# Kernel tuning notes

Measured on AMD Instinct MI355X. Metric: run time of the kernel, lower is better.

The kernel has to match this reference:

```python
import jax, jax.numpy as jnp
import numpy as np

B, DIM, T = 16, 128, 4096
CODEBOOK = 1024


def setup_inputs() -> dict:
    key = jax.random.key(0)
    k1, k2 = jax.random.split(key)
    x = jax.random.normal(k1, (B, DIM, T), dtype=jnp.float32)
    embed = jax.random.normal(k2, (CODEBOOK, DIM), dtype=jnp.float32) * 0.02
    return {"x": x, "embed": embed}


def reference(x, embed):
    Bq, D, Tq = x.shape
    n_codes = embed.shape[0]
    # [B, D, T] -> [B*T, D]
    x_flat = x.transpose(0, 2, 1).reshape(-1, D)
    d2 = (
        jnp.sum(x_flat * x_flat, axis=-1, keepdims=True)
        - 2.0 * (x_flat @ embed.T)
        + jnp.sum(embed * embed, axis=-1)[None, :]
    )  # [N, n_codes]
    indices = jnp.argmin(d2, axis=-1)  # [N]
    quantized = embed[indices]  # [N, D]
    # commitment_loss + codebook_loss: numerically both equal mse(x, q) in fwd
    diff = x_flat - quantized
    loss = 2.0 * jnp.mean(diff * diff)
    # straight-through value equals quantized in forward
    quantized_st = quantized.reshape(Bq, Tq, D).transpose(0, 2, 1)
    # utilization = fraction of codes used (jit-safe scatter instead of unique)
    used = jnp.zeros((n_codes,), jnp.float32).at[indices].set(1.0)
    utilization = jnp.sum(used) / n_codes
    return quantized_st, indices, loss, utilization
```

## Files before the change

kernel.cpp:

```cpp
#include <hip/hip_runtime.h>
#include <hip/hip_fp16.h>

#define B_ 16
#define D_ 128
#define T_ 4096
#define C_ 1024
#define N_ (B_*T_)
#define MARGIN 1.5e-3f

typedef __attribute__((ext_vector_type(8))) __fp16 fp16x8;
typedef __attribute__((ext_vector_type(4))) float f32x4;
typedef unsigned int u32;
typedef unsigned short u16;

static __device__ __forceinline__ fp16x8 as_fp16x8(int4 v) {
    union { int4 i; fp16x8 h; } u; u.i = v; return u.h;
}
static __device__ __forceinline__ u32 pack_h2(float a, float b) {
    return (u32)__half_as_ushort(__float2half(a)) |
           ((u32)__half_as_ushort(__float2half(b)) << 16);
}

__global__ __launch_bounds__(256) void vq_init_kernel(float* used, float* accum, int* nflag) {
    int tid = blockIdx.x * 256 + threadIdx.x;
    if (tid < C_) used[tid] = 0.0f;
    if (tid == 0) { accum[0] = 0.0f; nflag[0] = 0; }
}

__global__ __launch_bounds__(256) void vq_e2_kernel(const float* __restrict__ embed,
                                                    float* __restrict__ e2) {
#pragma clang fp contract(off)
    int c = blockIdx.x * 256 + threadIdx.x;
    const float* row = embed + (size_t)c * D_;
    float r[8];
#pragma unroll
    for (int j = 0; j < 8; ++j) { float v = row[j]; r[j] = v * v; }
    for (int i = 8; i < D_; i += 8) {
#pragma unroll
        for (int j = 0; j < 8; ++j) { float v = row[i + j]; r[j] = r[j] + v * v; }
    }
    e2[c] = ((r[0] + r[1]) + (r[2] + r[3])) + ((r[4] + r[5]) + (r[6] + r[7]));
}

__global__ __launch_bounds__(256) void vq_eprep_kernel(const float* __restrict__ embed,
                                                       u32* __restrict__ epk_hi,
                                                       u32* __restrict__ epk_lo,
                                                       float* __restrict__ eT) {
    int i = blockIdx.x * 256 + threadIdx.x;
    int c = i >> 6, d2 = i & 63;
    float2 v = reinterpret_cast<const float2*>(embed)[i];
    __half h0 = __float2half(v.x), h1 = __float2half(v.y);
    float l0 = v.x - __half2float(h0), l1 = v.y - __half2float(h1);
    u32 hp = (u32)__half_as_ushort(h0) | ((u32)__half_as_ushort(h1) << 16);
    u32 lp = (u32)__half_as_ushort(__float2half(l0)) |
             ((u32)__half_as_ushort(__float2half(l1)) << 16);
    int chunk = (c >> 6) * 16 + ((c >> 4) & 3) * 4 + (d2 >> 4);
    int oi = chunk * 256 + (((d2 >> 2) & 3) * 16 + (c & 15)) * 4 + (d2 & 3);
    epk_hi[oi] = hp;
    epk_lo[oi] = lp;
    int d0 = d2 * 2;
    eT[(size_t)d0 * C_ + c]       = v.x;
    eT[(size_t)(d0 + 1) * C_ + c] = v.y;
}

__global__ __launch_bounds__(256) void vq_mfma_kernel(
    const float* __restrict__ x, const u32* __restrict__ epk_hi, const u32* __restrict__ epk_lo,
    const float* __restrict__ e2, float* __restrict__ idx_f, int* __restrict__ idx_i,
    int* __restrict__ flagged, int* __restrict__ nflag)
{
    __shared__ int4  xb_lds[1024];
    __shared__ float mv1[4][64];
    __shared__ int   mi1[4][64];
    __shared__ float mv2[4][64];

    const int g  = blockIdx.x;
    const int b  = g >> 6;
    const int t0 = (g & 63) << 6;
    const int tid = threadIdx.x;
    const int w  = tid >> 6;
    const int l  = tid & 63;
    const int r  = l & 15;
    const int q  = l >> 4;

    {
        const int s = w;
        const float* xp = x + (size_t)b * ((size_t)D_ * T_) + (t0 + 16 * s + r);
#pragma unroll
        for (int t = 0; t < 4; ++t) {
            float f[8];
#pragma unroll
            for (int j = 0; j < 8; ++j)
                f[j] = xp[(size_t)(32 * t + 8 * q + j) * T_];
            int4 pk;
            pk.x = (int)pack_h2(f[0], f[1]);
            pk.y = (int)pack_h2(f[2], f[3]);
            pk.z = (int)pack_h2(f[4], f[5]);
            pk.w = (int)pack_h2(f[6], f[7]);
            xb_lds[(s * 4 + t) * 64 + l] = pk;
        }
    }
    __syncthreads();

    float rv1[4], rv2[4];
    int   ri1[4];
#pragma unroll
    for (int s = 0; s < 4; ++s) { rv1[s] = 3.4e38f; rv2[s] = 3.4e38f; ri1[s] = 0; }

    const u32* ephi = epk_hi + w * 1024 + l * 4;
    const u32* eplo = epk_lo + w * 1024 + l * 4;

    for (int rnd = 0; rnd < 16; ++rnd) {
        int4 eh4[4], el4[4];
#pragma unroll
        for (int t = 0; t < 4; ++t) {
            eh4[t] = *reinterpret_cast<const int4*>(ephi + rnd * 4096 + t * 256);
            el4[t] = *reinterpret_cast<const int4*>(eplo + rnd * 4096 + t * 256);
        }
        f32x4 eev = *reinterpret_cast<const f32x4*>(e2 + rnd * 64 + w * 16 + 4 * q);

#pragma unroll
        for (int s = 0; s < 4; ++s) {
            f32x4 acc = {0.f, 0.f, 0.f, 0.f};
#pragma unroll
            for (int t = 0; t < 4; ++t) {
                fp16x8 xa = as_fp16x8(xb_lds[(s * 4 + t) * 64 + l]);
                acc = __builtin_amdgcn_mfma_f32_16x16x32_f16(as_fp16x8(eh4[t]), xa, acc, 0, 0, 0);
                acc = __builtin_amdgcn_mfma_f32_16x16x32_f16(as_fp16x8(el4[t]), xa, acc, 0, 0, 0);
            }
#pragma unroll
            for (int reg = 0; reg < 4; ++reg) {
                float sc = fmaf(-2.0f, acc[reg], eev[reg]);
                int c = rnd * 64 + w * 16 + 4 * q + reg;
                if (sc < rv1[s]) { rv2[s] = rv1[s]; rv1[s] = sc; ri1[s] = c; }
                else rv2[s] = fminf(rv2[s], sc);
            }
        }
    }

#pragma unroll
    for (int s = 0; s < 4; ++s) {
        float v1 = rv1[s], v2 = rv2[s];
        int   i1 = ri1[s];
#pragma unroll
        for (int mo = 0; mo < 2; ++mo) {
            int m = 16 << mo;
            float ov1 = __shfl_xor(v1, m, 64);
            int   oi1 = __shfl_xor(i1, m, 64);
            float ov2 = __shfl_xor(v2, m, 64);
            float nv2 = fminf(fmaxf(v1, ov1), fminf(v2, ov2));
            if (ov1 < v1 || (ov1 == v1 && oi1 < i1)) { v1 = ov1; i1 = oi1; }
            v2 = nv2;
        }
        if (q == 0) { mv1[w][16 * s + r] = v1; mi1[w][16 * s + r] = i1; mv2[w][16 * s + r] = v2; }
    }
    __syncthreads();

    if (tid < 64) {
        float V1 = 3.4e38f, V2 = 3.4e38f;
        int   I1 = 0;
#pragma unroll
        for (int w2 = 0; w2 < 4; ++w2) {
            float a1 = mv1[w2][tid]; int ai = mi1[w2][tid]; float a2 = mv2[w2][tid];
            if (a1 < V1 || (a1 == V1 && ai < I1)) { V2 = fminf(V2, V1); V1 = a1; I1 = ai; }
            else V2 = fminf(V2, a1);
            V2 = fminf(V2, a2);
        }
        int n = g * 64 + tid;
        idx_i[n] = I1;
        idx_f[n] = (float)I1;
        if (V2 - V1 < MARGIN) { int pos = atomicAdd(nflag, 1); flagged[pos] = n; }
    }
}

__global__ __launch_bounds__(256) void vq_refine_kernel(
    const float* __restrict__ x, const float* __restrict__ eT,
    const float* __restrict__ e2,
    const int* __restrict__ flagged, const int* __restrict__ nflag,
    float* __restrict__ idx_f, int* __restrict__ idx_i)
{
    __shared__ float xs[D_];
    __shared__ float r8s[8];
    __shared__ float xxsh;
    __shared__ float wvv[4];
    __shared__ int   wvi[4];

    const int tid = threadIdx.x;
    const int wv_ = tid >> 6;
    const int l   = tid & 63;
    const int total = *nflag;

    for (int fi = blockIdx.x; fi < total; fi += gridDim.x) {
        __syncthreads();
        int n = flagged[fi];
        int b = n >> 12;
        int t = n & (T_ - 1);
        if (tid < D_) xs[tid] = x[(size_t)b * ((size_t)D_ * T_) + (size_t)tid * T_ + t];
        __syncthreads();

        if (tid < 8) {
#pragma clang fp contract(off)
            float v0 = xs[tid];
            float rj = v0 * v0;
            for (int i = 8; i < D_; i += 8) { float v = xs[i + tid]; rj = rj + v * v; }
            r8s[tid] = rj;
        }
        __syncthreads();
        if (tid == 0) {
#pragma clang fp contract(off)
            xxsh = ((r8s[0] + r8s[1]) + (r8s[2] + r8s[3])) + ((r8s[4] + r8s[5]) + (r8s[6] + r8s[7]));
        }
        __syncthreads();
        const float xx = xxsh;

        float acc0 = 0.f, acc1 = 0.f, acc2 = 0.f, acc3 = 0.f;
        const float* ep = eT + wv_ * 256 + l;
        for (int d = 0; d < D_; ++d) {
            float xv = xs[d];
            const float* rowp = ep + (size_t)d * C_;
            acc0 = fmaf(xv, rowp[0],   acc0);
            acc1 = fmaf(xv, rowp[64],  acc1);
            acc2 = fmaf(xv, rowp[128], acc2);
            acc3 = fmaf(xv, rowp[192], acc3);
        }

        float best = 3.4e38f;
        int   bi = 0;
        float a4[4] = {acc0, acc1, acc2, acc3};
#pragma unroll
        for (int k = 0; k < 4; ++k) {
            int c = wv_ * 256 + 64 * k + l;
            float s;
            {
#pragma clang fp contract(off)
                s = (xx - 2.0f * a4[k]) + e2[c];
            }
            if (s < best) { best = s; bi = c; }
        }
#pragma unroll
        for (int m = 1; m <= 32; m <<= 1) {
            float ov = __shfl_xor(best, m, 64);
            int   oc = __shfl_xor(bi, m, 64);
            if (ov < best || (ov == best && oc < bi)) { best = ov; bi = oc; }
        }
        if (l == 0) { wvv[wv_] = best; wvi[wv_] = bi; }
        __syncthreads();
        if (tid == 0) {
            float V = wvv[0]; int I = wvi[0];
#pragma unroll
            for (int w2 = 1; w2 < 4; ++w2) {
                if (wvv[w2] < V || (wvv[w2] == V && wvi[w2] < I)) { V = wvv[w2]; I = wvi[w2]; }
            }
            idx_i[n] = I;
            idx_f[n] = (float)I;
        }
    }
}

__global__ __launch_bounds__(256) void vq_gather_kernel(
    const float* __restrict__ x, const float* __restrict__ embed,
    const int* __restrict__ idx_i, float* __restrict__ out_q,
    float* __restrict__ accum, float* __restrict__ used)
{
    __shared__ int sidx[64];
    __shared__ float red[256];

    const int g  = blockIdx.x;
    const int b  = g >> 6;
    const int t0 = (g & 63) << 6;
    const int tid = threadIdx.x;

    if (tid < 64) {
        int ci = idx_i[g * 64 + tid];
        sidx[tid] = ci;
        used[ci] = 1.0f;
    }
    __syncthreads();

    const float* xb = x     + (size_t)b * ((size_t)D_ * T_) + t0;
    float*       ob = out_q + (size_t)b * ((size_t)D_ * T_) + t0;

    float local = 0.f;
#pragma unroll
    for (int k = 0; k < 32; ++k) {
        int e = tid + 256 * k;
        int d = e >> 6, tt = e & 63;
        float qv = embed[(size_t)sidx[tt] * D_ + d];
        float xv = xb[(size_t)d * T_ + tt];
        ob[(size_t)d * T_ + tt] = qv;
        float df = xv - qv;
        local += df * df;
    }

    red[tid] = local;
    __syncthreads();
    for (int st = 128; st > 0; st >>= 1) {
        if (tid < st) red[tid] += red[tid + st];
        __syncthreads();
    }
    if (tid == 0) atomicAdd(accum, red[0]);
}

__global__ __launch_bounds__(256) void vq_final_kernel(
    const float* __restrict__ used, const float* __restrict__ accum,
    float* __restrict__ out_loss, float* __restrict__ out_util)
{
    __shared__ float red[256];
    int tid = threadIdx.x;
    float s = 0.f;
    for (int k = tid; k < C_; k += 256) s += used[k];
    red[tid] = s;
    __syncthreads();
    for (int st = 128; st > 0; st >>= 1) {
        if (tid < st) red[tid] += red[tid + st];
        __syncthreads();
    }
    if (tid == 0) {
        out_loss[0] = 2.0f * accum[0] / (float)((size_t)N_ * D_);
        out_util[0] = red[0] / (float)C_;
    }
}

extern "C" void kernel_launch(void* const* d_in, const int* in_sizes, int n_in,
                              void* d_out, int out_size, void* d_ws, size_t ws_size,
                              hipStream_t stream) {
    const float* x     = (const float*)d_in[0];
    const float* embed = (const float*)d_in[1];

    float* out      = (float*)d_out;
    float* out_q    = out;
    float* idx_f    = out + (size_t)B_ * D_ * T_;
    float* out_loss = idx_f + N_;
    float* out_util = out_loss + 1;

    float* ws      = (float*)d_ws;
    float* e2      = ws;
    float* used    = ws + 1024;
    int*   idx_i   = (int*)(ws + 2048);
    float* accum   = ws + 67584;
    int*   nflag   = (int*)(ws + 67585);
    int*   flagged = (int*)(ws + 67588);
    u32*   epk_hi  = (u32*)(ws + 133124);
    u32*   epk_lo  = (u32*)(ws + 198660);
    float* eT      = ws + 264196;

    vq_init_kernel  <<<4, 256, 0, stream>>>(used, accum, nflag);
    vq_e2_kernel    <<<C_ / 256, 256, 0, stream>>>(embed, e2);
    vq_eprep_kernel <<<C_ * D_ / 2 / 256, 256, 0, stream>>>(embed, epk_hi, epk_lo, eT);
    vq_mfma_kernel  <<<N_ / 64, 256, 0, stream>>>(x, epk_hi, epk_lo, e2, idx_f, idx_i, flagged, nflag);
    vq_refine_kernel<<<1024, 256, 0, stream>>>(x, eT, e2, flagged, nflag, idx_f, idx_i);
    vq_gather_kernel<<<N_ / 64, 256, 0, stream>>>(x, embed, idx_i, out_q, accum, used);
    vq_final_kernel <<<1, 256, 0, stream>>>(used, accum, out_loss, out_util);
}
```

Before: 113.0 us.

## Keep x fragments in registers and batch refine over multiple flagged rows

In the MFMA kernel, each wave now loads and converts all four 16-column x tiles into registers instead of staging one tile per wave through LDS. The codebook fragments are loaded once per round and reused across all four tiles, with launch bounds and s_setprio added around the MFMA burst. The refine kernel handles 8 flagged rows per block, so each eT load is reused across 8 dot products, and its grid shrinks from 1024 to 256 blocks. The cost is higher register pressure, which may reduce occupancy, and redundant x loads because every wave now reads the whole 64-column tile.

```diff
diff --git a/kernel.cpp b/kernel.cpp
--- a/kernel.cpp
+++ b/kernel.cpp
@@ -7,6 +7,7 @@
 #define C_ 1024
 #define N_ (B_*T_)
 #define MARGIN 1.5e-3f
+#define RB 8
 
 typedef __attribute__((ext_vector_type(8))) __fp16 fp16x8;
 typedef __attribute__((ext_vector_type(4))) float f32x4;
@@ -63,12 +64,11 @@
     eT[(size_t)(d0 + 1) * C_ + c] = v.y;
 }
 
-__global__ __launch_bounds__(256) void vq_mfma_kernel(
+__global__ __launch_bounds__(256, 4) void vq_mfma_kernel(
     const float* __restrict__ x, const u32* __restrict__ epk_hi, const u32* __restrict__ epk_lo,
     const float* __restrict__ e2, float* __restrict__ idx_f, int* __restrict__ idx_i,
     int* __restrict__ flagged, int* __restrict__ nflag)
 {
-    __shared__ int4  xb_lds[1024];
     __shared__ float mv1[4][64];
     __shared__ int   mi1[4][64];
     __shared__ float mv2[4][64];
@@ -82,24 +82,26 @@
     const int r  = l & 15;
     const int q  = l >> 4;
 
+    fp16x8 xh[4][4];
     {
-        const int s = w;
-        const float* xp = x + (size_t)b * ((size_t)D_ * T_) + (t0 + 16 * s + r);
-#pragma unroll
-        for (int t = 0; t < 4; ++t) {
-            float f[8];
-#pragma unroll
-            for (int j = 0; j < 8; ++j)
-                f[j] = xp[(size_t)(32 * t + 8 * q + j) * T_];
-            int4 pk;
-            pk.x = (int)pack_h2(f[0], f[1]);
-            pk.y = (int)pack_h2(f[2], f[3]);
-            pk.z = (int)pack_h2(f[4], f[5]);
-            pk.w = (int)pack_h2(f[6], f[7]);
-            xb_lds[(s * 4 + t) * 64 + l] = pk;
-        }
-    }
-    __syncthreads();
+        const float* xp = x + (size_t)b * ((size_t)D_ * T_) + t0 + r;
+#pragma unroll
+        for (int s = 0; s < 4; ++s) {
+#pragma unroll
+            for (int t = 0; t < 4; ++t) {
+                float f[8];
+#pragma unroll
+                for (int j = 0; j < 8; ++j)
+                    f[j] = xp[16 * s + (size_t)(32 * t + 8 * q + j) * T_];
+                int4 pk;
+                pk.x = (int)pack_h2(f[0], f[1]);
+                pk.y = (int)pack_h2(f[2], f[3]);
+                pk.z = (int)pack_h2(f[4], f[5]);
+                pk.w = (int)pack_h2(f[6], f[7]);
+                xh[s][t] = as_fp16x8(pk);
+            }
+        }
+    }
 
     float rv1[4], rv2[4];
     int   ri1[4];
@@ -108,29 +110,34 @@
 
     const u32* ephi = epk_hi + w * 1024 + l * 4;
     const u32* eplo = epk_lo + w * 1024 + l * 4;
+    const int cbaseq = w * 16 + 4 * q;
 
     for (int rnd = 0; rnd < 16; ++rnd) {
-        int4 eh4[4], el4[4];
+        f32x4 eev = *reinterpret_cast<const f32x4*>(e2 + rnd * 64 + cbaseq);
+        f32x4 acc[4];
+#pragma unroll
+        for (int s = 0; s < 4; ++s) acc[s] = f32x4{0.f, 0.f, 0.f, 0.f};
+
+        __builtin_amdgcn_s_setprio(1);
 #pragma unroll
         for (int t = 0; t < 4; ++t) {
-            eh4[t] = *reinterpret_cast<const int4*>(ephi + rnd * 4096 + t * 256);
-            el4[t] = *reinterpret_cast<const int4*>(eplo + rnd * 4096 + t * 256);
-        }
-        f32x4 eev = *reinterpret_cast<const f32x4*>(e2 + rnd * 64 + w * 16 + 4 * q);
+            int4 eh = *reinterpret_cast<const int4*>(ephi + t * 256);
+            int4 el = *reinterpret_cast<const int4*>(eplo + t * 256);
+#pragma unroll
+            for (int s = 0; s < 4; ++s) {
+                acc[s] = __builtin_amdgcn_mfma_f32_16x16x32_f16(as_fp16x8(eh), xh[s][t], acc[s], 0, 0, 0);
+                acc[s] = __builtin_amdgcn_mfma_f32_16x16x32_f16(as_fp16x8(el), xh[s][t], acc[s], 0, 0, 0);
+            }
+        }
+        __builtin_amdgcn_s_setprio(0);
+        ephi += 4096; eplo += 4096;
 
 #pragma unroll
         for (int s = 0; s < 4; ++s) {
-            f32x4 acc = {0.f, 0.f, 0.f, 0.f};
-#pragma unroll
-            for (int t = 0; t < 4; ++t) {
-                fp16x8 xa = as_fp16x8(xb_lds[(s * 4 + t) * 64 + l]);
-                acc = __builtin_amdgcn_mfma_f32_16x16x32_f16(as_fp16x8(eh4[t]), xa, acc, 0, 0, 0);
-                acc = __builtin_amdgcn_mfma_f32_16x16x32_f16(as_fp16x8(el4[t]), xa, acc, 0, 0, 0);
-            }
 #pragma unroll
             for (int reg = 0; reg < 4; ++reg) {
-                float sc = fmaf(-2.0f, acc[reg], eev[reg]);
-                int c = rnd * 64 + w * 16 + 4 * q + reg;
+                float sc = fmaf(-2.0f, acc[s][reg], eev[reg]);
+                int c = rnd * 64 + cbaseq + reg;
                 if (sc < rv1[s]) { rv2[s] = rv1[s]; rv1[s] = sc; ri1[s] = c; }
                 else rv2[s] = fminf(rv2[s], sc);
             }
@@ -178,80 +185,109 @@
     const int* __restrict__ flagged, const int* __restrict__ nflag,
     float* __restrict__ idx_f, int* __restrict__ idx_i)
 {
-    __shared__ float xs[D_];
-    __shared__ float r8s[8];
-    __shared__ float xxsh;
-    __shared__ float wvv[4];
-    __shared__ int   wvi[4];
+    __shared__ float xs[RB][D_];
+    __shared__ float r8s[RB][8];
+    __shared__ float xxs[RB];
+    __shared__ float wvv[RB][4];
+    __shared__ int   wvi[RB][4];
 
     const int tid = threadIdx.x;
     const int wv_ = tid >> 6;
     const int l   = tid & 63;
     const int total = *nflag;
 
-    for (int fi = blockIdx.x; fi < total; fi += gridDim.x) {
-        __syncthreads();
-        int n = flagged[fi];
-        int b = n >> 12;
-        int t = n & (T_ - 1);
-        if (tid < D_) xs[tid] = x[(size_t)b * ((size_t)D_ * T_) + (size_t)tid * T_ + t];
-        __syncthreads();
-
-        if (tid < 8) {
+    for (int base = blockIdx.x * RB; base < total; base += gridDim.x * RB) {
+        __syncthreads();
+#pragma unroll
+        for (int e = 0; e < RB * D_ / 256; ++e) {
+            int idx = tid + e * 256;
+            int k = idx >> 7, d = idx & 127;
+            float v = 0.f;
+            int fi = base + k;
+            if (fi < total) {
+                int n = flagged[fi];
+                int bb = n >> 12, t = n & (T_ - 1);
+                v = x[(size_t)bb * ((size_t)D_ * T_) + (size_t)d * T_ + t];
+            }
+            xs[k][d] = v;
+        }
+        __syncthreads();
+
+        if (tid < RB * 8) {
 #pragma clang fp contract(off)
-            float v0 = xs[tid];
+            int k = tid >> 3, j = tid & 7;
+            float v0 = xs[k][j];
             float rj = v0 * v0;
-            for (int i = 8; i < D_; i += 8) { float v = xs[i + tid]; rj = rj + v * v; }
-            r8s[tid] = rj;
-        }
-        __syncthreads();
-        if (tid == 0) {
+            for (int i = 8; i < D_; i += 8) { float v = xs[k][i + j]; rj = rj + v * v; }
+            r8s[k][j] = rj;
+        }
+        __syncthreads();
+        if (tid < RB) {
 #pragma clang fp contract(off)
-            xxsh = ((r8s[0] + r8s[1]) + (r8s[2] + r8s[3])) + ((r8s[4] + r8s[5]) + (r8s[6] + r8s[7]));
-        }
-        __syncthreads();
-        const float xx = xxsh;
-
-        float acc0 = 0.f, acc1 = 0.f, acc2 = 0.f, acc3 = 0.f;
+            xxs[tid] = ((r8s[tid][0] + r8s[tid][1]) + (r8s[tid][2] + r8s[tid][3]))
+                     + ((r8s[tid][4] + r8s[tid][5]) + (r8s[tid][6] + r8s[tid][7]));
+        }
+        __syncthreads();
+
+        float acc[4][RB];
+#pragma unroll
+        for (int k2 = 0; k2 < 4; ++k2)
+#pragma unroll
+            for (int k = 0; k < RB; ++k) acc[k2][k] = 0.f;
+
         const float* ep = eT + wv_ * 256 + l;
         for (int d = 0; d < D_; ++d) {
-            float xv = xs[d];
             const float* rowp = ep + (size_t)d * C_;
-            acc0 = fmaf(xv, rowp[0],   acc0);
-            acc1 = fmaf(xv, rowp[64],  acc1);
-            acc2 = fmaf(xv, rowp[128], acc2);
-            acc3 = fmaf(xv, rowp[192], acc3);
-        }
-
-        float best = 3.4e38f;
-        int   bi = 0;
-        float a4[4] = {acc0, acc1, acc2, acc3};
-#pragma unroll
-        for (int k = 0; k < 4; ++k) {
-            int c = wv_ * 256 + 64 * k + l;
-            float s;
-            {
+            float ev0 = rowp[0], ev1 = rowp[64], ev2 = rowp[128], ev3 = rowp[192];
+#pragma unroll
+            for (int k = 0; k < RB; ++k) {
+                float xv = xs[k][d];
+                acc[0][k] = fmaf(xv, ev0, acc[0][k]);
+                acc[1][k] = fmaf(xv, ev1, acc[1][k]);
+                acc[2][k] = fmaf(xv, ev2, acc[2][k]);
+                acc[3][k] = fmaf(xv, ev3, acc[3][k]);
+            }
+        }
+
+        float e2v[4];
+#pragma unroll
+        for (int k2 = 0; k2 < 4; ++k2) e2v[k2] = e2[wv_ * 256 + 64 * k2 + l];
+
+#pragma unroll
+        for (int k = 0; k < RB; ++k) {
+            float xx = xxs[k];
+            float best = 3.4e38f;
+            int   bi = 0;
+#pragma unroll
+            for (int k2 = 0; k2 < 4; ++k2) {
+                int c = wv_ * 256 + 64 * k2 + l;
+                float s;
+                {
 #pragma clang fp contract(off)
-                s = (xx - 2.0f * a4[k]) + e2[c];
-            }
-            if (s < best) { best = s; bi = c; }
-        }
-#pragma unroll
-        for (int m = 1; m <= 32; m <<= 1) {
-            float ov = __shfl_xor(best, m, 64);
-            int   oc = __shfl_xor(bi, m, 64);
-            if (ov < best || (ov == best && oc < bi)) { best = ov; bi = oc; }
-        }
-        if (l == 0) { wvv[wv_] = best; wvi[wv_] = bi; }
-        __syncthreads();
-        if (tid == 0) {
-            float V = wvv[0]; int I = wvi[0];
-#pragma unroll
-            for (int w2 = 1; w2 < 4; ++w2) {
-                if (wvv[w2] < V || (wvv[w2] == V && wvi[w2] < I)) { V = wvv[w2]; I = wvi[w2]; }
-            }
-            idx_i[n] = I;
-            idx_f[n] = (float)I;
+                    s = (xx - 2.0f * acc[k2][k]) + e2v[k2];
+                }
+                if (s < best) { best = s; bi = c; }
+            }
+#pragma unroll
+            for (int m = 1; m <= 32; m <<= 1) {
+                float ov = __shfl_xor(best, m, 64);
+                int   oc = __shfl_xor(bi, m, 64);
+                if (ov < best || (ov == best && oc < bi)) { best = ov; bi = oc; }
+            }
+            if (l == 0) { wvv[k][wv_] = best; wvi[k][wv_] = bi; }
+        }
+        __syncthreads();
+        if (tid < RB) {
+            int k = tid;
+            if (base + k < total) {
+                float V = wvv[k][0]; int I = wvi[k][0];
+#pragma unroll
+                for (int w2 = 1; w2 < 4; ++w2)
+                    if (wvv[k][w2] < V || (wvv[k][w2] == V && wvi[k][w2] < I)) { V = wvv[k][w2]; I = wvi[k][w2]; }
+                int n = flagged[base + k];
+                idx_i[n] = I;
+                idx_f[n] = (float)I;
+            }
         }
     }
 }
@@ -347,7 +383,7 @@
     vq_e2_kernel    <<<C_ / 256, 256, 0, stream>>>(embed, e2);
     vq_eprep_kernel <<<C_ * D_ / 2 / 256, 256, 0, stream>>>(embed, epk_hi, epk_lo, eT);
     vq_mfma_kernel  <<<N_ / 64, 256, 0, stream>>>(x, epk_hi, epk_lo, e2, idx_f, idx_i, flagged, nflag);
-    vq_refine_kernel<<<1024, 256, 0, stream>>>(x, eT, e2, flagged, nflag, idx_f, idx_i);
+    vq_refine_kernel<<<256, 256, 0, stream>>>(x, eT, e2, flagged, nflag, idx_f, idx_i);
     vq_gather_kernel<<<N_ / 64, 256, 0, stream>>>(x, embed, idx_i, out_q, accum, used);
     vq_final_kernel <<<1, 256, 0, stream>>>(used, accum, out_loss, out_util);
 }
```

Measured after the change: 124.5 us. 1.1x slower.
